# Kernel optimization log

Measured on AMD Instinct MI355X. Metric: run time of the kernel, lower is better.

The kernel has to match this reference:

```python
import jax, jax.numpy as jnp
import numpy as np

N, E, D, H = 100000, 400000, 128, 128  # nodes, edges, feat dim, mlp hidden


def _ln(x, g, b, eps=1e-5):
    m = jnp.mean(x, axis=-1, keepdims=True)
    v = jnp.mean((x - m) ** 2, axis=-1, keepdims=True)
    return (x - m) * jax.lax.rsqrt(v + eps) * g + b


def _mlp(x, w0, b0, w1, b1, w2, b2):
    # Linear->ReLU->Linear->ReLU->Linear (last act = Identity)
    h = jax.nn.relu(x @ w0 + b0)
    h = jax.nn.relu(h @ w1 + b1)
    return h @ w2 + b2


def setup_inputs() -> dict:
    key = jax.random.key(0)
    ks = jax.random.split(key, 16)
    node_x = jax.random.normal(ks[0], (N, D), dtype=jnp.float32)
    edge_attr = jax.random.normal(ks[1], (E, D), dtype=jnp.float32)
    edge_index = jax.random.randint(ks[2], (2, E), 0, N, dtype=jnp.int32)

    def lin(k, fin, fout):
        kw, kb = jax.random.split(k)
        s = 1.0 / np.sqrt(fin)
        w = jax.random.uniform(kw, (fin, fout), jnp.float32, -s, s)
        b = jax.random.uniform(kb, (fout,), jnp.float32, -s, s)
        return w, b

    # message MLP: (3D) -> H -> H -> D, then LayerNorm(D)
    msg_w0, msg_b0 = lin(ks[3], 3 * D, H)
    msg_w1, msg_b1 = lin(ks[4], H, H)
    msg_w2, msg_b2 = lin(ks[5], H, D)
    # top-level update MLP: (D + D) -> H -> H -> D, then LayerNorm(D)
    upd_w0, upd_b0 = lin(ks[6], 2 * D, H)
    upd_w1, upd_b1 = lin(ks[7], H, H)
    upd_w2, upd_b2 = lin(ks[8], H, D)
    return {
        "node_x": node_x, "edge_attr": edge_attr, "edge_index": edge_index,
        "msg_w0": msg_w0, "msg_b0": msg_b0, "msg_w1": msg_w1, "msg_b1": msg_b1,
        "msg_w2": msg_w2, "msg_b2": msg_b2,
        "msg_g": jnp.ones((D,), jnp.float32), "msg_beta": jnp.zeros((D,), jnp.float32),
        "upd_w0": upd_w0, "upd_b0": upd_b0, "upd_w1": upd_w1, "upd_b1": upd_b1,
        "upd_w2": upd_w2, "upd_b2": upd_b2,
        "upd_g": jnp.ones((D,), jnp.float32), "upd_beta": jnp.zeros((D,), jnp.float32),
    }


def reference(node_x, edge_attr, edge_index,
              msg_w0, msg_b0, msg_w1, msg_b1, msg_w2, msg_b2, msg_g, msg_beta,
              upd_w0, upd_b0, upd_w1, upd_b1, upd_w2, upd_b2, upd_g, upd_beta):
    src, dst = edge_index[0], edge_index[1]
    # PyG default flow source_to_target: x_j = x[src], x_i = x[dst]
    x_i = node_x[dst]                       # [E, D]
    x_j = node_x[src]                       # [E, D]
    concat = jnp.concatenate([x_i, x_j, edge_attr], axis=1)  # [E, 3D]
    msg = _ln(_mlp(concat, msg_w0, msg_b0, msg_w1, msg_b1, msg_w2, msg_b2), msg_g, msg_beta)
    new_edge = edge_attr + msg              # edge_attr[:] += msg in original
    # scatter-add messages onto target nodes
    agg = jax.ops.segment_sum(new_edge, dst, num_segments=N)  # [N, D]
    concat2 = jnp.concatenate([node_x, agg], axis=1)          # [N, 2D]
    upd = _ln(_mlp(concat2, upd_w0, upd_b0, upd_w1, upd_b1, upd_w2, upd_b2), upd_g, upd_beta)
    return node_x + upd
```

## Files before the change

### kernel.cpp

```cpp
#include <hip/hip_runtime.h>

typedef __attribute__((ext_vector_type(4))) float f32x4;
typedef __attribute__((ext_vector_type(8))) __bf16 bf16x8;

constexpr int FD = 128;

__device__ __forceinline__ uint4 pack8(const float* v) {
  union { __bf16 h[8]; uint4 u; } cv;
#pragma unroll
  for (int q = 0; q < 8; ++q) cv.h[q] = (__bf16)v[q];
  return cv.u;
}
__device__ __forceinline__ unsigned int pack2(float a, float b) {
  union { __bf16 h[2]; unsigned int u; } cv;
  cv.h[0] = (__bf16)a; cv.h[1] = (__bf16)b;
  return cv.u;
}

__global__ void cvt_bf16(const float* __restrict__ x, unsigned short* __restrict__ o, int n8) {
  int i = blockIdx.x * 256 + threadIdx.x;
  if (i >= n8) return;
  const float* p = x + (size_t)i * 8;
  float v[8];
#pragma unroll
  for (int q = 0; q < 8; ++q) v[q] = p[q];
  *(uint4*)(o + (size_t)i * 8) = pack8(v);
}

__global__ void pack_weights(const float* __restrict__ mw0, const float* __restrict__ mw1,
                             const float* __restrict__ mw2, const float* __restrict__ uw0,
                             const float* __restrict__ uw1, const float* __restrict__ uw2,
                             unsigned short* __restrict__ wp) {
  int tid = blockIdx.x * 256 + threadIdx.x;
  const float* src; int base, K;
  if      (tid < 49152)  { src = mw0; base = 0;      K = 384; }
  else if (tid < 65536)  { src = mw1; base = 49152;  K = 128; }
  else if (tid < 81920)  { src = mw2; base = 65536;  K = 128; }
  else if (tid < 114688) { src = uw0; base = 81920;  K = 256; }
  else if (tid < 131072) { src = uw1; base = 114688; K = 128; }
  else                   { src = uw2; base = 131072; K = 128; }
  int i = tid - base;
  int k = i >> 7, n = i & 127;
  int KS = K >> 5;
  int dst = base + (((n >> 4) * KS + (k >> 5)) * 64 + ((k >> 3) & 3) * 16 + (n & 15)) * 8 + (k & 7);
  union { __bf16 h; unsigned short s; } cv; cv.h = (__bf16)src[i];
  wp[dst] = cv.s;
}


__global__ __launch_bounds__(512, 6)
void in_edge_kernel(const float* __restrict__ node_x, const unsigned short* __restrict__ nxbf,
                    const float* __restrict__ edge_attr,
                    const int* __restrict__ eidx, const unsigned short* __restrict__ wp,
                    const float* __restrict__ b0p, const float* __restrict__ b1p,
                    const float* __restrict__ b2p, const float* __restrict__ gp,
                    const float* __restrict__ bep,
                    unsigned short* __restrict__ msg, int* __restrict__ head,
                    int* __restrict__ nxt, float* __restrict__ agg,
                    int use_sort, int E) {
  __shared__ unsigned short sBuf[3072 * 8];
  __shared__ int sSrc[64], sDst[64];
  __shared__ float sG[128], sB[128];

  const int t = threadIdx.x;
  const int e0 = blockIdx.x * 64;
  const int lane = t & 63, w = t >> 6;
  const int ln = lane & 15, g16 = lane >> 4;
  const int rg = w & 1;
  const int cg = w >> 1;
  const int nt0 = cg * 2, nt1 = cg * 2 + 1;
  const int rdoff = ln * 32 + g16 * 8;
  const int stf = cg * 2048 + g16 * 128 + (ln & 7);
  const int perm0 = (((ln >> 3)) & 3) * 8;
  const int perm1 = ((2 + (ln >> 3)) & 3) * 8;

  bf16x8 BA[8];
#pragma unroll
  for (int k = 0; k < 4; ++k) {
    BA[k]     = *(const bf16x8*)(wp + (size_t)((nt0 * 12 + k) * 64 + lane) * 8);
    BA[4 + k] = *(const bf16x8*)(wp + (size_t)((nt1 * 12 + k) * 64 + lane) * 8);
  }

  if (t < 64) {
    sSrc[t] = (e0 + t < E) ? eidx[e0 + t] : 0;
  } else if (t < 128) {
    int r = t - 64;
    int e = e0 + r;
    int d = (e < E) ? eidx[E + e] : 0;
    sDst[r] = d;
    if (use_sort && e < E) nxt[e] = atomicExch(&head[d], e);
  } else if (t < 256) {
    sG[t - 128] = gp[t - 128];
  } else if (t < 384) {
    sB[t - 256] = bep[t - 256];
  }
  __syncthreads();

  if (nxbf) {
#pragma unroll
    for (int it = 0; it < 2; ++it) {
      int f = t + it * 512;
      int row = f >> 4, j = f & 15;
      uint4 v = {0, 0, 0, 0}, u = {0, 0, 0, 0};
      if (e0 + row < E) {
        v = *(const uint4*)(nxbf + (size_t)sDst[row] * FD + j * 8);
        u = *(const uint4*)(nxbf + (size_t)sSrc[row] * FD + j * 8);
      }
      int c = (((j >> 2) * 4 + (row >> 4)) * 64 + (row & 15) * 4 + (j & 3)) * 8;
      *(uint4*)&sBuf[c] = v;
      *(uint4*)&sBuf[c + 8192] = u;
    }
  } else {
#pragma unroll
    for (int it = 0; it < 16; ++it) {
      const int type = it >> 3;
      int row = ((it & 7) << 3) + w;
      float2 v = {0.f, 0.f};
      if (e0 + row < E) {
        const float* sp = (type == 0) ? node_x + (size_t)sDst[row] * FD
                                      : node_x + (size_t)sSrc[row] * FD;
        v = *(const float2*)(sp + lane * 2);
      }
      int c = (((type * 4 + (lane >> 4)) * 4 + (row >> 4)) * 64
               + (row & 15) * 4 + ((lane >> 2) & 3)) * 8 + (lane & 3) * 2;
      *(unsigned int*)&sBuf[c] = pack2(v.x, v.y);
    }
  }
#pragma unroll
  for (int it = 0; it < 8; ++it) {
    int row = it * 8 + w;
    float2 v = {0.f, 0.f};
    if (e0 + row < E) v = *(const float2*)(edge_attr + (size_t)(e0 + row) * FD + lane * 2);
    int c = 16384 + (((lane >> 4) * 4 + (row >> 4)) * 64
                     + (row & 15) * 4 + ((lane >> 2) & 3)) * 8 + (lane & 3) * 2;
    *(unsigned int*)&sBuf[c] = pack2(v.x, v.y);
  }
  __syncthreads();

  const float b0A = b0p[cg * 32 + ln],      b0B = b0p[cg * 32 + 16 + ln];
  const float b1A = b1p[cg * 32 + ln],      b1B = b1p[cg * 32 + 16 + ln];
  const float b2A = b2p[cg * 32 + ln],      b2B = b2p[cg * 32 + 16 + ln];

  f32x4 acc[2][2];
#pragma unroll
  for (int mi = 0; mi < 2; ++mi)
#pragma unroll
    for (int nj = 0; nj < 2; ++nj) acc[mi][nj] = (f32x4){0.f, 0.f, 0.f, 0.f};

#pragma unroll
  for (int ks = 0; ks < 12; ++ks) {
    bf16x8 bbA = BA[ks & 3];
    bf16x8 bbB = BA[4 + (ks & 3)];
    if (ks + 4 < 12) {
      BA[ks & 3]       = *(const bf16x8*)(wp + (size_t)((nt0 * 12 + ks + 4) * 64 + lane) * 8);
      BA[4 + (ks & 3)] = *(const bf16x8*)(wp + (size_t)((nt1 * 12 + ks + 4) * 64 + lane) * 8);
    }
#pragma unroll
    for (int mi = 0; mi < 2; ++mi) {
      bf16x8 a = *(const bf16x8*)&sBuf[(ks * 4 + rg * 2 + mi) * 512 + rdoff];
      acc[mi][0] = __builtin_amdgcn_mfma_f32_16x16x32_bf16(a, bbA, acc[mi][0], 0, 0, 0);
      acc[mi][1] = __builtin_amdgcn_mfma_f32_16x16x32_bf16(a, bbB, acc[mi][1], 0, 0, 0);
    }
  }
#pragma unroll
  for (int k = 0; k < 4; ++k) {
    BA[k]     = *(const bf16x8*)(wp + 49152 + (size_t)((nt0 * 4 + k) * 64 + lane) * 8);
    BA[4 + k] = *(const bf16x8*)(wp + 49152 + (size_t)((nt1 * 4 + k) * 64 + lane) * 8);
  }
  __syncthreads();

#pragma unroll
  for (int mi = 0; mi < 2; ++mi)
#pragma unroll
    for (int ri = 0; ri < 4; ++ri) {
      union { __bf16 h; unsigned short s; } c0, c1;
      c0.h = (__bf16)fmaxf(acc[mi][0][ri] + b0A, 0.f);
      c1.h = (__bf16)fmaxf(acc[mi][1][ri] + b0B, 0.f);
      int o = (rg * 2 + mi) * 512 + ri * 32 + stf;
      sBuf[o + perm0] = c0.s;
      sBuf[o + perm1] = c1.s;
      acc[mi][0][ri] = 0.f; acc[mi][1][ri] = 0.f;
    }
  __syncthreads();

#pragma unroll
  for (int ks = 0; ks < 4; ++ks)
#pragma unroll
    for (int mi = 0; mi < 2; ++mi) {
      bf16x8 a = *(const bf16x8*)&sBuf[(ks * 4 + rg * 2 + mi) * 512 + rdoff];
      acc[mi][0] = __builtin_amdgcn_mfma_f32_16x16x32_bf16(a, BA[ks], acc[mi][0], 0, 0, 0);
      acc[mi][1] = __builtin_amdgcn_mfma_f32_16x16x32_bf16(a, BA[4 + ks], acc[mi][1], 0, 0, 0);
    }
#pragma unroll
  for (int k = 0; k < 4; ++k) {
    BA[k]     = *(const bf16x8*)(wp + 65536 + (size_t)((nt0 * 4 + k) * 64 + lane) * 8);
    BA[4 + k] = *(const bf16x8*)(wp + 65536 + (size_t)((nt1 * 4 + k) * 64 + lane) * 8);
  }
#pragma unroll
  for (int mi = 0; mi < 2; ++mi)
#pragma unroll
    for (int ri = 0; ri < 4; ++ri) {
      union { __bf16 h; unsigned short s; } c0, c1;
      c0.h = (__bf16)fmaxf(acc[mi][0][ri] + b1A, 0.f);
      c1.h = (__bf16)fmaxf(acc[mi][1][ri] + b1B, 0.f);
      int o = 8192 + (rg * 2 + mi) * 512 + ri * 32 + stf;
      sBuf[o + perm0] = c0.s;
      sBuf[o + perm1] = c1.s;
      acc[mi][0][ri] = 0.f; acc[mi][1][ri] = 0.f;
    }
  __syncthreads();

#pragma unroll
  for (int ks = 0; ks < 4; ++ks)
#pragma unroll
    for (int mi = 0; mi < 2; ++mi) {
      bf16x8 a = *(const bf16x8*)&sBuf[8192 + (ks * 4 + rg * 2 + mi) * 512 + rdoff];
      acc[mi][0] = __builtin_amdgcn_mfma_f32_16x16x32_bf16(a, BA[ks], acc[mi][0], 0, 0, 0);
      acc[mi][1] = __builtin_amdgcn_mfma_f32_16x16x32_bf16(a, BA[4 + ks], acc[mi][1], 0, 0, 0);
    }
#pragma unroll
  for (int mi = 0; mi < 2; ++mi)
#pragma unroll
    for (int ri = 0; ri < 4; ++ri) {
      union { __bf16 h; unsigned short s; } c0, c1;
      c0.h = (__bf16)(acc[mi][0][ri] + b2A);
      c1.h = (__bf16)(acc[mi][1][ri] + b2B);
      int o = (rg * 2 + mi) * 512 + ri * 32 + stf;
      sBuf[o + perm0] = c0.s;
      sBuf[o + perm1] = c1.s;
    }
  __syncthreads();

  {
    int row = t >> 3, j = t & 7;
    int a0 = (((j >> 1) * 4 + (row >> 4)) * 64 + (row & 15) * 4 + 2 * (j & 1)) * 8;
    bf16x8 v0 = *(const bf16x8*)&sBuf[a0];
    bf16x8 v1 = *(const bf16x8*)&sBuf[a0 + 8];
    float s1 = 0.f, s2 = 0.f;
#pragma unroll
    for (int q = 0; q < 8; ++q) {
      float a = (float)v0[q], b = (float)v1[q];
      s1 += a + b; s2 += a * a + b * b;
    }
#pragma unroll
    for (int m = 1; m < 8; m <<= 1) {
      s1 += __shfl_xor(s1, m, 64);
      s2 += __shfl_xor(s2, m, 64);
    }
    float mean = s1 * (1.f / 128.f);
    float var  = s2 * (1.f / 128.f) - mean * mean;
    float rstd = rsqrtf(fmaxf(var, 0.f) + 1e-5f);

    int e = e0 + row;
    if (e < E) {
      bf16x8 ea0 = *(const bf16x8*)&sBuf[a0 + 16384];
      bf16x8 ea1 = *(const bf16x8*)&sBuf[a0 + 16384 + 8];
      float val[16];
#pragma unroll
      for (int q = 0; q < 8; ++q) {
        val[q]     = ((float)v0[q] - mean) * rstd * sG[j * 16 + q]     + sB[j * 16 + q]     + (float)ea0[q];
        val[8 + q] = ((float)v1[q] - mean) * rstd * sG[j * 16 + 8 + q] + sB[j * 16 + 8 + q] + (float)ea1[q];
      }
      if (use_sort) {
        uint4* dst = (uint4*)(msg + (size_t)e * FD + j * 16);
        dst[0] = pack8(val);
        dst[1] = pack8(val + 8);
      } else {
        float* ap = agg + (size_t)sDst[row] * FD + j * 16;
#pragma unroll
        for (int q = 0; q < 16; ++q) atomicAdd(ap + q, val[q]);
      }
    }
  }
}

__global__ __launch_bounds__(512, 8)
void in_node_kernel(const float* __restrict__ node_x, const unsigned short* __restrict__ nxbf,
                    const unsigned short* __restrict__ msg, const int* __restrict__ head,
                    const int* __restrict__ nxt, const float* __restrict__ agg,
                    const unsigned short* __restrict__ wp,
                    const float* __restrict__ b0p, const float* __restrict__ b1p,
                    const float* __restrict__ b2p, const float* __restrict__ gp,
                    const float* __restrict__ bep, float* __restrict__ out,
                    int use_sort, int N) {
  __shared__ unsigned short sBuf[2048 * 8];
  __shared__ float sG[128], sB[128];

  const int t = threadIdx.x;
  const int r0 = blockIdx.x * 64;
  const int lane = t & 63, w = t >> 6;
  const int ln = lane & 15, g16 = lane >> 4;
  const int col = w * 16 + ln;
  const int rdoff = ln * 32 + g16 * 8;
  const int stoff = (w >> 1) * 2048 + g16 * 128
                  + (((2 * w) + (ln >> 3)) & 3) * 8 + (ln & 7);

  bf16x8 b0[4];
#pragma unroll
  for (int ks = 0; ks < 4; ++ks)
    b0[ks] = *(const bf16x8*)(wp + 81920 + (size_t)((w * 8 + ks) * 64 + lane) * 8);

  if (t < 128)      sG[t] = gp[t];
  else if (t < 256) sB[t - 128] = bep[t - 128];

  if (nxbf) {
#pragma unroll
    for (int it = 0; it < 2; ++it) {
      int f = t + it * 512;
      int row = f >> 4, j = f & 15;
      int r = r0 + row;
      uint4 v = {0, 0, 0, 0};
      if (r < N) v = *(const uint4*)(nxbf + (size_t)r * FD + j * 8);
      int c = (((j >> 2) * 4 + (row >> 4)) * 64 + (row & 15) * 4 + (j & 3)) * 8;
      *(uint4*)&sBuf[c] = v;
    }
  } else {
#pragma unroll
    for (int it = 0; it < 8; ++it) {
      int row = (it << 3) + w;
      int r = r0 + row;
      float2 v = {0.f, 0.f};
      if (r < N) v = *(const float2*)(node_x + (size_t)r * FD + lane * 2);
      int c = (((lane >> 4) * 4 + (row >> 4)) * 64
               + (row & 15) * 4 + ((lane >> 2) & 3)) * 8 + (lane & 3) * 2;
      *(unsigned int*)&sBuf[c] = pack2(v.x, v.y);
    }
  }

  {
    int row = t >> 3, j = t & 7;
    int node = r0 + row;
    float a[16];
#pragma unroll
    for (int q = 0; q < 16; ++q) a[q] = 0.f;
    if (node < N) {
      if (use_sort) {
        int e = head[node];
        while (e >= 0) {
          int ne = nxt[e];
          bf16x8 m0 = *(const bf16x8*)(msg + (size_t)e * FD + j * 16);
          bf16x8 m1 = *(const bf16x8*)(msg + (size_t)e * FD + j * 16 + 8);
#pragma unroll
          for (int q = 0; q < 8; ++q) { a[q] += (float)m0[q]; a[8 + q] += (float)m1[q]; }
          e = ne;
        }
      } else {
        const float* ap = agg + (size_t)node * FD + j * 16;
#pragma unroll
        for (int q4 = 0; q4 < 4; ++q4) {
          f32x4 u = *(const f32x4*)(ap + q4 * 4);
#pragma unroll
          for (int q = 0; q < 4; ++q) a[q4 * 4 + q] = u[q];
        }
      }
    }
    int c = 8192 + (((j >> 1) * 4 + (row >> 4)) * 64 + (row & 15) * 4 + 2 * (j & 1)) * 8;
    *(uint4*)&sBuf[c] = pack8(a);
    *(uint4*)&sBuf[c + 8] = pack8(a + 8);
  }
  __syncthreads();

  const float b0v = b0p[col], b1v = b1p[col], b2v = b2p[col];

  f32x4 acc[4];
#pragma unroll
  for (int m = 0; m < 4; ++m) acc[m] = (f32x4){0.f, 0.f, 0.f, 0.f};

#pragma unroll
  for (int ks = 0; ks < 8; ++ks) {
    bf16x8 bb = b0[ks % 4];
    if (ks + 4 < 8)
      b0[ks % 4] = *(const bf16x8*)(wp + 81920 + (size_t)((w * 8 + ks + 4) * 64 + lane) * 8);
#pragma unroll
    for (int m = 0; m < 4; ++m) {
      bf16x8 a = *(const bf16x8*)&sBuf[(ks * 4 + m) * 512 + rdoff];
      acc[m] = __builtin_amdgcn_mfma_f32_16x16x32_bf16(a, bb, acc[m], 0, 0, 0);
    }
  }
  bf16x8 B1r[4];
#pragma unroll
  for (int ks = 0; ks < 4; ++ks)
    B1r[ks] = *(const bf16x8*)(wp + 114688 + (size_t)((w * 4 + ks) * 64 + lane) * 8);

  __syncthreads();
#pragma unroll
  for (int m = 0; m < 4; ++m)
#pragma unroll
    for (int ri = 0; ri < 4; ++ri) {
      union { __bf16 h; unsigned short s; } cv;
      cv.h = (__bf16)fmaxf(acc[m][ri] + b0v, 0.f);
      sBuf[stoff + m * 512 + ri * 32] = cv.s;
      acc[m][ri] = 0.f;
    }
  __syncthreads();

#pragma unroll
  for (int ks = 0; ks < 4; ++ks)
#pragma unroll
    for (int m = 0; m < 4; ++m) {
      bf16x8 a = *(const bf16x8*)&sBuf[(ks * 4 + m) * 512 + rdoff];
      acc[m] = __builtin_amdgcn_mfma_f32_16x16x32_bf16(a, B1r[ks], acc[m], 0, 0, 0);
    }
  bf16x8 B2r[4];
#pragma unroll
  for (int ks = 0; ks < 4; ++ks)
    B2r[ks] = *(const bf16x8*)(wp + 131072 + (size_t)((w * 4 + ks) * 64 + lane) * 8);
#pragma unroll
  for (int m = 0; m < 4; ++m)
#pragma unroll
    for (int ri = 0; ri < 4; ++ri) {
      union { __bf16 h; unsigned short s; } cv;
      cv.h = (__bf16)fmaxf(acc[m][ri] + b1v, 0.f);
      sBuf[8192 + stoff + m * 512 + ri * 32] = cv.s;
      acc[m][ri] = 0.f;
    }
  __syncthreads();

#pragma unroll
  for (int ks = 0; ks < 4; ++ks)
#pragma unroll
    for (int m = 0; m < 4; ++m) {
      bf16x8 a = *(const bf16x8*)&sBuf[8192 + (ks * 4 + m) * 512 + rdoff];
      acc[m] = __builtin_amdgcn_mfma_f32_16x16x32_bf16(a, B2r[ks], acc[m], 0, 0, 0);
    }
#pragma unroll
  for (int m = 0; m < 4; ++m)
#pragma unroll
    for (int ri = 0; ri < 4; ++ri) {
      union { __bf16 h; unsigned short s; } cv;
      cv.h = (__bf16)(acc[m][ri] + b2v);
      sBuf[stoff + m * 512 + ri * 32] = cv.s;
    }
  __syncthreads();

  {
    int row = t >> 3, j = t & 7;
    int a0 = (((j >> 1) * 4 + (row >> 4)) * 64 + (row & 15) * 4 + 2 * (j & 1)) * 8;
    bf16x8 v0 = *(const bf16x8*)&sBuf[a0];
    bf16x8 v1 = *(const bf16x8*)&sBuf[a0 + 8];
    float s1 = 0.f, s2 = 0.f;
#pragma unroll
    for (int q = 0; q < 8; ++q) {
      float a = (float)v0[q], b = (float)v1[q];
      s1 += a + b; s2 += a * a + b * b;
    }
#pragma unroll
    for (int m = 1; m < 8; m <<= 1) {
      s1 += __shfl_xor(s1, m, 64);
      s2 += __shfl_xor(s2, m, 64);
    }
    float mean = s1 * (1.f / 128.f);
    float var  = s2 * (1.f / 128.f) - mean * mean;
    float rstd = rsqrtf(fmaxf(var, 0.f) + 1e-5f);

    int node = r0 + row;
    if (node < N) {
      float o[16];
#pragma unroll
      for (int q = 0; q < 8; ++q) {
        o[q]     = ((float)v0[q] - mean) * rstd * sG[j * 16 + q]     + sB[j * 16 + q];
        o[8 + q] = ((float)v1[q] - mean) * rstd * sG[j * 16 + 8 + q] + sB[j * 16 + 8 + q];
      }
      const float* xr = node_x + (size_t)node * FD + j * 16;
      float* orow = out + (size_t)node * FD + j * 16;
#pragma unroll
      for (int q4 = 0; q4 < 4; ++q4) {
        f32x4 x = *(const f32x4*)(xr + q4 * 4);
        f32x4 wv;
#pragma unroll
        for (int q = 0; q < 4; ++q) wv[q] = o[q4 * 4 + q] + x[q];
        *(f32x4*)(orow + q4 * 4) = wv;
      }
    }
  }
}

extern "C" void kernel_launch(void* const* d_in, const int* in_sizes, int n_in,
                              void* d_out, int out_size, void* d_ws, size_t ws_size,
                              hipStream_t stream) {
  const float* node_x    = (const float*)d_in[0];
  const float* edge_attr = (const float*)d_in[1];
  const int*   eidx      = (const int*)d_in[2];
  const int N = in_sizes[0] / FD;
  const int E = in_sizes[1] / FD;

  char* ws = (char*)d_ws;
  auto aln = [](size_t x) { return (x + 255) & ~(size_t)255; };
  const size_t wpB   = aln(294912);
  const size_t nxbfB = aln((size_t)N * FD * 2);
  const size_t headB = aln((size_t)N * 4);
  const size_t nxtB  = aln((size_t)E * 4);
  const size_t msgB  = (size_t)E * FD * 2;

  unsigned short* wp = (unsigned short*)ws;
  unsigned short* nxbf = nullptr;
  int* head = nullptr; int* nxt = nullptr;
  unsigned short* msg = nullptr; float* agg = nullptr;
  int use_sort = 0;

  if (ws_size >= wpB + nxbfB + headB + nxtB + msgB) {
    use_sort = 1;
    nxbf = (unsigned short*)(ws + wpB);
    head = (int*)(ws + wpB + nxbfB);
    nxt  = (int*)(ws + wpB + nxbfB + headB);
    msg  = (unsigned short*)(ws + wpB + nxbfB + headB + nxtB);
  } else if (ws_size >= wpB + headB + nxtB + msgB) {
    use_sort = 1;
    head = (int*)(ws + wpB);
    nxt  = (int*)(ws + wpB + headB);
    msg  = (unsigned short*)(ws + wpB + headB + nxtB);
  } else {
    agg = (float*)(ws + wpB);
  }

  if (use_sort) (void)hipMemsetAsync(head, 0xFF, (size_t)N * 4, stream);
  else          (void)hipMemsetAsync(agg, 0, (size_t)N * FD * sizeof(float), stream);

  pack_weights<<<576, 256, 0, stream>>>(
      (const float*)d_in[3], (const float*)d_in[5], (const float*)d_in[7],
      (const float*)d_in[11], (const float*)d_in[13], (const float*)d_in[15], wp);
  if (nxbf) cvt_bf16<<<(N * FD / 8 + 255) / 256, 256, 0, stream>>>(node_x, nxbf, N * FD / 8);
  in_edge_kernel<<<(E + 63) / 64, 512, 0, stream>>>(
      node_x, nxbf, edge_attr, eidx, wp,
      (const float*)d_in[4], (const float*)d_in[6], (const float*)d_in[8],
      (const float*)d_in[9], (const float*)d_in[10],
      msg, head, nxt, agg, use_sort, E);
  in_node_kernel<<<(N + 63) / 64, 512, 0, stream>>>(
      node_x, nxbf, msg, head, nxt, agg, wp,
      (const float*)d_in[12], (const float*)d_in[14], (const float*)d_in[16],
      (const float*)d_in[17], (const float*)d_in[18], (float*)d_out, use_sort, N);
}
```

Measured before the change: 245.0 us.

## Shrink edge-kernel tile to 32 edges with 4 waves and add MFMA priority hints

```diff
diff --git a/kernel.cpp b/kernel.cpp
--- a/kernel.cpp
+++ b/kernel.cpp
@@ -48,7 +48,7 @@
 }
 
 
-__global__ __launch_bounds__(512, 6)
+__global__ __launch_bounds__(256, 6)
 void in_edge_kernel(const float* __restrict__ node_x, const unsigned short* __restrict__ nxbf,
                     const float* __restrict__ edge_attr,
                     const int* __restrict__ eidx, const unsigned short* __restrict__ wp,
@@ -58,21 +58,19 @@
                     unsigned short* __restrict__ msg, int* __restrict__ head,
                     int* __restrict__ nxt, float* __restrict__ agg,
                     int use_sort, int E) {
-  __shared__ unsigned short sBuf[3072 * 8];
-  __shared__ int sSrc[64], sDst[64];
+  __shared__ unsigned short sBuf[3 * 4096];
+  __shared__ int sSrc[32], sDst[32];
   __shared__ float sG[128], sB[128];
 
   const int t = threadIdx.x;
-  const int e0 = blockIdx.x * 64;
+  const int e0 = blockIdx.x * 32;
   const int lane = t & 63, w = t >> 6;
   const int ln = lane & 15, g16 = lane >> 4;
-  const int rg = w & 1;
-  const int cg = w >> 1;
-  const int nt0 = cg * 2, nt1 = cg * 2 + 1;
+  const int nt0 = w * 2, nt1 = w * 2 + 1;
   const int rdoff = ln * 32 + g16 * 8;
-  const int stf = cg * 2048 + g16 * 128 + (ln & 7);
-  const int perm0 = (((ln >> 3)) & 3) * 8;
-  const int perm1 = ((2 + (ln >> 3)) & 3) * 8;
+  const int perm0 = (ln >> 3) * 8;
+  const int perm1 = (2 + (ln >> 3)) * 8;
+  const int stf = (g16 * 4) * 32 + (ln & 7);
 
   bf16x8 BA[8];
 #pragma unroll
@@ -81,65 +79,60 @@
     BA[4 + k] = *(const bf16x8*)(wp + (size_t)((nt1 * 12 + k) * 64 + lane) * 8);
   }
 
-  if (t < 64) {
+  if (t < 32) {
     sSrc[t] = (e0 + t < E) ? eidx[e0 + t] : 0;
-  } else if (t < 128) {
-    int r = t - 64;
-    int e = e0 + r;
+  } else if (t < 64) {
+    int r = t - 32, e = e0 + r;
     int d = (e < E) ? eidx[E + e] : 0;
     sDst[r] = d;
     if (use_sort && e < E) nxt[e] = atomicExch(&head[d], e);
-  } else if (t < 256) {
-    sG[t - 128] = gp[t - 128];
-  } else if (t < 384) {
-    sB[t - 256] = bep[t - 256];
-  }
+  }
+  if (t < 128)      sG[t] = gp[t];
+  else              sB[t - 128] = bep[t - 128];
   __syncthreads();
 
   if (nxbf) {
 #pragma unroll
-    for (int it = 0; it < 2; ++it) {
-      int f = t + it * 512;
+    for (int it = 0; it < 4; ++it) {
+      int f = (t + it * 256) & 511;
       int row = f >> 4, j = f & 15;
-      uint4 v = {0, 0, 0, 0}, u = {0, 0, 0, 0};
-      if (e0 + row < E) {
-        v = *(const uint4*)(nxbf + (size_t)sDst[row] * FD + j * 8);
-        u = *(const uint4*)(nxbf + (size_t)sSrc[row] * FD + j * 8);
-      }
-      int c = (((j >> 2) * 4 + (row >> 4)) * 64 + (row & 15) * 4 + (j & 3)) * 8;
+      const int* idx = (it < 2) ? sDst : sSrc;
+      int tb = (it < 2) ? 0 : 4096;
+      uint4 v = {0, 0, 0, 0};
+      if (e0 + row < E) v = *(const uint4*)(nxbf + (size_t)idx[row] * FD + j * 8);
+      int c = tb + ((j >> 2) * 2 + (row >> 4)) * 512 + (row & 15) * 32 + (j & 3) * 8;
       *(uint4*)&sBuf[c] = v;
-      *(uint4*)&sBuf[c + 8192] = u;
     }
   } else {
 #pragma unroll
     for (int it = 0; it < 16; ++it) {
       const int type = it >> 3;
-      int row = ((it & 7) << 3) + w;
+      int row = (it & 7) * 4 + w;
       float2 v = {0.f, 0.f};
       if (e0 + row < E) {
         const float* sp = (type == 0) ? node_x + (size_t)sDst[row] * FD
                                       : node_x + (size_t)sSrc[row] * FD;
         v = *(const float2*)(sp + lane * 2);
       }
-      int c = (((type * 4 + (lane >> 4)) * 4 + (row >> 4)) * 64
-               + (row & 15) * 4 + ((lane >> 2) & 3)) * 8 + (lane & 3) * 2;
+      int c = type * 4096 + ((lane >> 4) * 2 + (row >> 4)) * 512
+            + (row & 15) * 32 + ((lane >> 2) & 3) * 8 + (lane & 3) * 2;
       *(unsigned int*)&sBuf[c] = pack2(v.x, v.y);
     }
   }
 #pragma unroll
   for (int it = 0; it < 8; ++it) {
-    int row = it * 8 + w;
+    int row = it * 4 + w;
     float2 v = {0.f, 0.f};
     if (e0 + row < E) v = *(const float2*)(edge_attr + (size_t)(e0 + row) * FD + lane * 2);
-    int c = 16384 + (((lane >> 4) * 4 + (row >> 4)) * 64
-                     + (row & 15) * 4 + ((lane >> 2) & 3)) * 8 + (lane & 3) * 2;
+    int c = 8192 + ((lane >> 4) * 2 + (row >> 4)) * 512
+          + (row & 15) * 32 + ((lane >> 2) & 3) * 8 + (lane & 3) * 2;
     *(unsigned int*)&sBuf[c] = pack2(v.x, v.y);
   }
   __syncthreads();
 
-  const float b0A = b0p[cg * 32 + ln],      b0B = b0p[cg * 32 + 16 + ln];
-  const float b1A = b1p[cg * 32 + ln],      b1B = b1p[cg * 32 + 16 + ln];
-  const float b2A = b2p[cg * 32 + ln],      b2B = b2p[cg * 32 + 16 + ln];
+  const float b0A = b0p[w * 32 + ln], b0B = b0p[w * 32 + 16 + ln];
+  const float b1A = b1p[w * 32 + ln], b1B = b1p[w * 32 + 16 + ln];
+  const float b2A = b2p[w * 32 + ln], b2B = b2p[w * 32 + 16 + ln];
 
   f32x4 acc[2][2];
 #pragma unroll
@@ -147,21 +140,23 @@
 #pragma unroll
     for (int nj = 0; nj < 2; ++nj) acc[mi][nj] = (f32x4){0.f, 0.f, 0.f, 0.f};
 
+  __builtin_amdgcn_s_setprio(1);
 #pragma unroll
   for (int ks = 0; ks < 12; ++ks) {
-    bf16x8 bbA = BA[ks & 3];
-    bf16x8 bbB = BA[4 + (ks & 3)];
+    bf16x8 bbA = BA[ks & 3], bbB = BA[4 + (ks & 3)];
     if (ks + 4 < 12) {
       BA[ks & 3]       = *(const bf16x8*)(wp + (size_t)((nt0 * 12 + ks + 4) * 64 + lane) * 8);
       BA[4 + (ks & 3)] = *(const bf16x8*)(wp + (size_t)((nt1 * 12 + ks + 4) * 64 + lane) * 8);
     }
+    int tb = (ks >> 2) * 4096, kl = ks & 3;
 #pragma unroll
     for (int mi = 0; mi < 2; ++mi) {
-      bf16x8 a = *(const bf16x8*)&sBuf[(ks * 4 + rg * 2 + mi) * 512 + rdoff];
+      bf16x8 a = *(const bf16x8*)&sBuf[tb + (kl * 2 + mi) * 512 + rdoff];
       acc[mi][0] = __builtin_amdgcn_mfma_f32_16x16x32_bf16(a, bbA, acc[mi][0], 0, 0, 0);
       acc[mi][1] = __builtin_amdgcn_mfma_f32_16x16x32_bf16(a, bbB, acc[mi][1], 0, 0, 0);
     }
   }
+  __builtin_amdgcn_s_setprio(0);
 #pragma unroll
   for (int k = 0; k < 4; ++k) {
     BA[k]     = *(const bf16x8*)(wp + 49152 + (size_t)((nt0 * 4 + k) * 64 + lane) * 8);
@@ -176,21 +171,23 @@
       union { __bf16 h; unsigned short s; } c0, c1;
       c0.h = (__bf16)fmaxf(acc[mi][0][ri] + b0A, 0.f);
       c1.h = (__bf16)fmaxf(acc[mi][1][ri] + b0B, 0.f);
-      int o = (rg * 2 + mi) * 512 + ri * 32 + stf;
+      int o = (w * 2 + mi) * 512 + ri * 32 + stf;
       sBuf[o + perm0] = c0.s;
       sBuf[o + perm1] = c1.s;
       acc[mi][0][ri] = 0.f; acc[mi][1][ri] = 0.f;
     }
   __syncthreads();
 
+  __builtin_amdgcn_s_setprio(1);
 #pragma unroll
   for (int ks = 0; ks < 4; ++ks)
 #pragma unroll
     for (int mi = 0; mi < 2; ++mi) {
-      bf16x8 a = *(const bf16x8*)&sBuf[(ks * 4 + rg * 2 + mi) * 512 + rdoff];
+      bf16x8 a = *(const bf16x8*)&sBuf[(ks * 2 + mi) * 512 + rdoff];
       acc[mi][0] = __builtin_amdgcn_mfma_f32_16x16x32_bf16(a, BA[ks], acc[mi][0], 0, 0, 0);
       acc[mi][1] = __builtin_amdgcn_mfma_f32_16x16x32_bf16(a, BA[4 + ks], acc[mi][1], 0, 0, 0);
     }
+  __builtin_amdgcn_s_setprio(0);
 #pragma unroll
   for (int k = 0; k < 4; ++k) {
     BA[k]     = *(const bf16x8*)(wp + 65536 + (size_t)((nt0 * 4 + k) * 64 + lane) * 8);
@@ -203,21 +200,23 @@
       union { __bf16 h; unsigned short s; } c0, c1;
       c0.h = (__bf16)fmaxf(acc[mi][0][ri] + b1A, 0.f);
       c1.h = (__bf16)fmaxf(acc[mi][1][ri] + b1B, 0.f);
-      int o = 8192 + (rg * 2 + mi) * 512 + ri * 32 + stf;
+      int o = 4096 + (w * 2 + mi) * 512 + ri * 32 + stf;
       sBuf[o + perm0] = c0.s;
       sBuf[o + perm1] = c1.s;
       acc[mi][0][ri] = 0.f; acc[mi][1][ri] = 0.f;
     }
   __syncthreads();
 
+  __builtin_amdgcn_s_setprio(1);
 #pragma unroll
   for (int ks = 0; ks < 4; ++ks)
 #pragma unroll
     for (int mi = 0; mi < 2; ++mi) {
-      bf16x8 a = *(const bf16x8*)&sBuf[8192 + (ks * 4 + rg * 2 + mi) * 512 + rdoff];
+      bf16x8 a = *(const bf16x8*)&sBuf[4096 + (ks * 2 + mi) * 512 + rdoff];
       acc[mi][0] = __builtin_amdgcn_mfma_f32_16x16x32_bf16(a, BA[ks], acc[mi][0], 0, 0, 0);
       acc[mi][1] = __builtin_amdgcn_mfma_f32_16x16x32_bf16(a, BA[4 + ks], acc[mi][1], 0, 0, 0);
     }
+  __builtin_amdgcn_s_setprio(0);
 #pragma unroll
   for (int mi = 0; mi < 2; ++mi)
 #pragma unroll
@@ -225,7 +224,7 @@
       union { __bf16 h; unsigned short s; } c0, c1;
       c0.h = (__bf16)(acc[mi][0][ri] + b2A);
       c1.h = (__bf16)(acc[mi][1][ri] + b2B);
-      int o = (rg * 2 + mi) * 512 + ri * 32 + stf;
+      int o = (w * 2 + mi) * 512 + ri * 32 + stf;
       sBuf[o + perm0] = c0.s;
       sBuf[o + perm1] = c1.s;
     }
@@ -233,7 +232,7 @@
 
   {
     int row = t >> 3, j = t & 7;
-    int a0 = (((j >> 1) * 4 + (row >> 4)) * 64 + (row & 15) * 4 + 2 * (j & 1)) * 8;
+    int a0 = ((j >> 1) * 2 + (row >> 4)) * 512 + (row & 15) * 32 + (j & 1) * 16;
     bf16x8 v0 = *(const bf16x8*)&sBuf[a0];
     bf16x8 v1 = *(const bf16x8*)&sBuf[a0 + 8];
     float s1 = 0.f, s2 = 0.f;
@@ -253,8 +252,8 @@
 
     int e = e0 + row;
     if (e < E) {
-      bf16x8 ea0 = *(const bf16x8*)&sBuf[a0 + 16384];
-      bf16x8 ea1 = *(const bf16x8*)&sBuf[a0 + 16384 + 8];
+      bf16x8 ea0 = *(const bf16x8*)&sBuf[8192 + a0];
+      bf16x8 ea1 = *(const bf16x8*)&sBuf[8192 + a0 + 8];
       float val[16];
 #pragma unroll
       for (int q = 0; q < 8; ++q) {
@@ -520,7 +519,7 @@
       (const float*)d_in[3], (const float*)d_in[5], (const float*)d_in[7],
       (const float*)d_in[11], (const float*)d_in[13], (const float*)d_in[15], wp);
   if (nxbf) cvt_bf16<<<(N * FD / 8 + 255) / 256, 256, 0, stream>>>(node_x, nxbf, N * FD / 8);
-  in_edge_kernel<<<(E + 63) / 64, 512, 0, stream>>>(
+  in_edge_kernel<<<(E + 31) / 32, 256, 0, stream>>>(
       node_x, nxbf, edge_attr, eidx, wp,
       (const float*)d_in[4], (const float*)d_in[6], (const float*)d_in[8],
       (const float*)d_in[9], (const float*)d_in[10],
```

After: 262.0 us. 1.07x slower.
